# Optimization experiments

Hardware: AMD Instinct MI355X
Metric: run time of the kernel (lower is better)

Reference implementation:

```python
import jax, jax.numpy as jnp
import numpy as np

H = 1024   # hidden_size
A = 16     # number_ab (branches)
O = 4      # num_outputs per branch
B = 4096   # batch
P = 2048   # number of selected rows
EPS = 1e-5


def setup_inputs() -> dict:
    key = jax.random.key(0)
    ks = jax.random.split(key, 12)
    s = 0.02  # weight init scale
    inp = {
        "X": jax.random.normal(ks[0], (B, H), jnp.float32),
        "X1": jax.random.normal(ks[1], (B, H), jnp.float32),
        # stacked per-branch parameters (batched over antibody axis A)
        "W1": jax.random.normal(ks[2], (A, H, H), jnp.float32) * s,
        "b1": jnp.zeros((A, H), jnp.float32),
        "W2": jax.random.normal(ks[3], (A, H, H), jnp.float32) * s,
        "b2": jnp.zeros((A, H), jnp.float32),
        "W3": jax.random.normal(ks[4], (A, H, H), jnp.float32) * s,
        "b3": jnp.zeros((A, H), jnp.float32),
        "gamma": jnp.ones((A, H), jnp.float32),
        "beta": jnp.zeros((A, H), jnp.float32),
        "W4": jax.random.normal(ks[5], (A, H, O), jnp.float32) * s,
        "b4": jnp.zeros((A, O), jnp.float32),
        "positions_y": jax.random.randint(ks[6], (P,), 0, B, jnp.int32),
    }
    return inp


def reference(X, X1, W1, b1, W2, b2, W3, b3, gamma, beta, W4, b4, positions_y):
    # z = l1(X) + l2(X1) per branch, batched over A: [B, A, H]
    z = (jnp.einsum('bh,aho->bao', X, W1) + b1
         + jnp.einsum('bh,aho->bao', X1, W2) + b2)
    # mlm: Linear -> ReLU -> LayerNorm -> Linear
    h = jax.nn.relu(jnp.einsum('bah,aho->bao', z, W3) + b3)  # [B, A, H]
    mu = jnp.mean(h, axis=-1, keepdims=True)
    var = jnp.var(h, axis=-1, keepdims=True)  # biased, matches nn.LayerNorm
    hn = (h - mu) / jnp.sqrt(var + EPS) * gamma + beta
    y = jnp.einsum('bah,aho->bao', hn, W4) + b4  # [B, A, O]
    # torch.cat along dim 1 over branches -> [B, A*O]
    Y = y.reshape(B, A * O)
    return Y[positions_y]
```

## Files before the change

### kernel.cpp

```cpp
#include <hip/hip_runtime.h>
#include <hip/hip_bf16.h>

using bf16 = __hip_bfloat16;
typedef __bf16 v8bf __attribute__((ext_vector_type(8)));
typedef float v4f __attribute__((ext_vector_type(4)));

#define H_ 1024
#define A_ 16
#define O_ 4
#define B_ 4096
#define P_ 2048
#define EPS_ 1e-5f

__device__ __forceinline__ void gl_lds16(const void* g, void* l) {
    __builtin_amdgcn_global_load_lds(
        (const __attribute__((address_space(1))) void*)g,
        (__attribute__((address_space(3))) void*)l, 16, 0, 0);
}

__global__ void addbias_k(const float* __restrict__ b1, const float* __restrict__ b2,
                          float* __restrict__ b12, int n) {
    int i = blockIdx.x * 256 + threadIdx.x;
    if (i < n) b12[i] = b1[i] + b2[i];
}

__global__ __launch_bounds__(256) void gather_k(const float* __restrict__ X,
                                                const float* __restrict__ X1,
                                                const int* __restrict__ pos,
                                                bf16* __restrict__ XX) {
    int p = blockIdx.x;
    int row = pos[p];
    const float4* x  = (const float4*)(X  + (size_t)row * H_);
    const float4* x1 = (const float4*)(X1 + (size_t)row * H_);
    bf16* o = XX + (size_t)p * (2 * H_);
    int i = threadIdx.x;
    float4 v = x[i];
    __align__(8) bf16 t[4];
    t[0] = __float2bfloat16(v.x); t[1] = __float2bfloat16(v.y);
    t[2] = __float2bfloat16(v.z); t[3] = __float2bfloat16(v.w);
    *(uint2*)(o + i * 4) = *(const uint2*)t;
    float4 w = x1[i];
    t[0] = __float2bfloat16(w.x); t[1] = __float2bfloat16(w.y);
    t[2] = __float2bfloat16(w.z); t[3] = __float2bfloat16(w.w);
    *(uint2*)(o + H_ + i * 4) = *(const uint2*)t;
}

__global__ __launch_bounds__(256) void transpose3_k(const float* __restrict__ W1s,
                                                    const float* __restrict__ W2s,
                                                    const float* __restrict__ W3s,
                                                    bf16* __restrict__ WT12,
                                                    bf16* __restrict__ WT3) {
    __shared__ float tile[64][65];
    const int which = blockIdx.z >> 4;
    const int a = blockIdx.z & 15;
    const float* src = (which == 0) ? W1s : (which == 1) ? W2s : W3s;
    bf16* dstBase = (which == 2) ? WT3 : WT12;
    const int dstK = (which == 2) ? H_ : 2 * H_;
    const int kOff = (which == 1) ? H_ : 0;

    const int k0 = blockIdx.x * 64;
    const int n0 = blockIdx.y * 64;
    const float* s = src + (size_t)a * H_ * H_;
    const int tc = threadIdx.x & 15;
    const int tr = threadIdx.x >> 4;
#pragma unroll
    for (int r = 0; r < 64; r += 16) {
        float4 v = *(const float4*)(s + (size_t)(k0 + tr + r) * H_ + n0 + tc * 4);
        tile[tr + r][tc * 4 + 0] = v.x;
        tile[tr + r][tc * 4 + 1] = v.y;
        tile[tr + r][tc * 4 + 2] = v.z;
        tile[tr + r][tc * 4 + 3] = v.w;
    }
    __syncthreads();
    bf16* d = dstBase + (size_t)a * H_ * dstK + kOff;
    const int wc = threadIdx.x & 7;
    const int wr = threadIdx.x >> 3;
#pragma unroll
    for (int r = 0; r < 64; r += 32) {
        const int n = wr + r;
        __align__(16) bf16 tmp[8];
#pragma unroll
        for (int j = 0; j < 8; j++) tmp[j] = __float2bfloat16(tile[wc * 8 + j][n]);
        *(uint4*)(d + (size_t)(n0 + n) * dstK + k0 + wc * 8) = *(const uint4*)tmp;
    }
}

template <bool RELU>
__global__ __launch_bounds__(256) void gemm_bt(const bf16* __restrict__ Amat, size_t aStrideA,
                                               const bf16* __restrict__ Bt,
                                               const float* __restrict__ bias,
                                               bf16* __restrict__ C,
                                               int M, int N, int K) {
    constexpr int BM = 128, BN = 128, BK = 32;
    __shared__ __align__(16) unsigned short As[2 * BM * BK];
    __shared__ __align__(16) unsigned short Bs[2 * BN * BK];

    const int L = blockIdx.x + 16 * blockIdx.y + 128 * blockIdx.z;
    const int xcd = L & 7;
    const int g = L >> 3;
    const int bm = g & 15;
    const int bna = xcd + 8 * (g >> 4);
    const int bn = bna & 7;
    const int a = bna >> 3;

    const bf16* Ab = Amat + (size_t)a * aStrideA;
    const bf16* Bb = Bt + (size_t)a * (size_t)N * K;
    const int tid = threadIdx.x;
    const int lane = tid & 63;
    const int wave = tid >> 6;
    const int wm = (wave & 1) * 64;
    const int wn = (wave >> 1) * 64;

    v4f acc[4][4];
#pragma unroll
    for (int i = 0; i < 4; i++)
#pragma unroll
        for (int j = 0; j < 4; j++) acc[i][j] = (v4f){0.f, 0.f, 0.f, 0.f};

    const int r0 = tid >> 2;
    const int cs = (((tid & 3) ^ ((r0 >> 1) & 3))) * 8;
    const bf16* agBase = Ab + (size_t)(bm * BM + r0) * K + cs;
    const bf16* bgBase = Bb + (size_t)(bn * BN + r0) * K + cs;
    const size_t rowSkip = (size_t)64 * K;
    const int w512 = wave * 512;

    const int lr = lane & 15;
    const int q = lane >> 4;
    const int kq = (q ^ ((lr >> 1) & 3)) * 8;

    const int nk = K / BK;

    {
        unsigned short* aB = As;
        unsigned short* bB = Bs;
        gl_lds16(agBase, aB + w512);
        gl_lds16(agBase + rowSkip, aB + 2048 + w512);
        gl_lds16(bgBase, bB + w512);
        gl_lds16(bgBase + rowSkip, bB + 2048 + w512);
    }

    for (int kt = 0; kt < nk; ++kt) {
        __syncthreads();
        if (kt + 1 < nk) {
            const int k0 = (kt + 1) * BK;
            unsigned short* aB = As + ((kt + 1) & 1) * 4096;
            unsigned short* bB = Bs + ((kt + 1) & 1) * 4096;
            gl_lds16(agBase + k0, aB + w512);
            gl_lds16(agBase + k0 + rowSkip, aB + 2048 + w512);
            gl_lds16(bgBase + k0, bB + w512);
            gl_lds16(bgBase + k0 + rowSkip, bB + 2048 + w512);
        }
        const unsigned short* Ar = As + (kt & 1) * 4096;
        const unsigned short* Br = Bs + (kt & 1) * 4096;
        v8bf af[4], bfr[4];
#pragma unroll
        for (int mi = 0; mi < 4; mi++)
            af[mi] = *(const v8bf*)(Ar + (wm + mi * 16 + lr) * BK + kq);
#pragma unroll
        for (int ni = 0; ni < 4; ni++)
            bfr[ni] = *(const v8bf*)(Br + (wn + ni * 16 + lr) * BK + kq);
#pragma unroll
        for (int mi = 0; mi < 4; mi++)
#pragma unroll
            for (int ni = 0; ni < 4; ni++)
                acc[mi][ni] = __builtin_amdgcn_mfma_f32_16x16x32_bf16(af[mi], bfr[ni],
                                                                      acc[mi][ni], 0, 0, 0);
    }

    const int lq = lane >> 4;
    bf16* Cb = C + (size_t)a * M * N;
#pragma unroll
    for (int ni = 0; ni < 4; ni++) {
        const int col = bn * BN + wn + ni * 16 + lr;
        const float bv = bias[(size_t)a * N + col];
#pragma unroll
        for (int mi = 0; mi < 4; mi++) {
            const int row0 = bm * BM + wm + mi * 16 + lq * 4;
#pragma unroll
            for (int rg = 0; rg < 4; rg++) {
                float v = acc[mi][ni][rg] + bv;
                if (RELU) v = v > 0.f ? v : 0.f;
                Cb[(size_t)(row0 + rg) * N + col] = __float2bfloat16(v);
            }
        }
    }
}

__global__ __launch_bounds__(256) void ln_head_k(const bf16* __restrict__ Hb,
                                                 const float* __restrict__ gamma,
                                                 const float* __restrict__ beta,
                                                 const float* __restrict__ W4,
                                                 const float* __restrict__ b4,
                                                 float* __restrict__ out) {
    int w = blockIdx.x * 4 + (threadIdx.x >> 6);
    int lane = threadIdx.x & 63;
    int a = w >> 11;
    int p = w & (P_ - 1);
    const bf16* hrow = Hb + ((size_t)a * P_ + p) * H_;
    float hv[16];
    float s = 0.f, ss = 0.f;
#pragma unroll
    for (int i = 0; i < 16; i++) {
        float v = __bfloat162float(hrow[lane + i * 64]);
        hv[i] = v;
        s += v;
        ss += v * v;
    }
#pragma unroll
    for (int off = 32; off; off >>= 1) {
        s += __shfl_xor(s, off);
        ss += __shfl_xor(ss, off);
    }
    float mu = s * (1.f / H_);
    float var = ss * (1.f / H_) - mu * mu;
    float rstd = rsqrtf(var + EPS_);
    const float* g = gamma + (size_t)a * H_;
    const float* be = beta + (size_t)a * H_;
    const float4* w4 = (const float4*)(W4 + (size_t)a * H_ * O_);
    float a0 = 0.f, a1 = 0.f, a2 = 0.f, a3 = 0.f;
#pragma unroll
    for (int i = 0; i < 16; i++) {
        int k = lane + i * 64;
        float hn = (hv[i] - mu) * rstd * g[k] + be[k];
        float4 wv = w4[k];
        a0 += hn * wv.x;
        a1 += hn * wv.y;
        a2 += hn * wv.z;
        a3 += hn * wv.w;
    }
#pragma unroll
    for (int off = 32; off; off >>= 1) {
        a0 += __shfl_xor(a0, off);
        a1 += __shfl_xor(a1, off);
        a2 += __shfl_xor(a2, off);
        a3 += __shfl_xor(a3, off);
    }
    if (lane < 4) {
        float v = (lane == 0 ? a0 : lane == 1 ? a1 : lane == 2 ? a2 : a3) + b4[a * O_ + lane];
        out[(size_t)p * (A_ * O_) + a * O_ + lane] = v;
    }
}

extern "C" void kernel_launch(void* const* d_in, const int* in_sizes, int n_in,
                              void* d_out, int out_size, void* d_ws, size_t ws_size,
                              hipStream_t stream) {
    const float* X     = (const float*)d_in[0];
    const float* X1    = (const float*)d_in[1];
    const float* W1    = (const float*)d_in[2];
    const float* b1    = (const float*)d_in[3];
    const float* W2    = (const float*)d_in[4];
    const float* b2    = (const float*)d_in[5];
    const float* W3    = (const float*)d_in[6];
    const float* b3    = (const float*)d_in[7];
    const float* gamma = (const float*)d_in[8];
    const float* beta  = (const float*)d_in[9];
    const float* W4    = (const float*)d_in[10];
    const float* b4    = (const float*)d_in[11];
    const int* pos     = (const int*)d_in[12];
    float* out = (float*)d_out;

    char* ws = (char*)d_ws;
    bf16* XX   = (bf16*)(ws);
    bf16* Z    = (bf16*)(ws + ((size_t)8 << 20));
    bf16* WT3  = (bf16*)(ws + ((size_t)72 << 20));
    bf16* WT12 = (bf16*)(ws + ((size_t)104 << 20));
    float* b12 = (float*)(ws + ((size_t)168 << 20));
    bf16* Hb   = WT12;

    addbias_k<<<(A_ * H_ + 255) / 256, 256, 0, stream>>>(b1, b2, b12, A_ * H_);
    gather_k<<<P_, 256, 0, stream>>>(X, X1, pos, XX);
    dim3 tgrid(H_ / 64, H_ / 64, 3 * A_);
    transpose3_k<<<tgrid, 256, 0, stream>>>(W1, W2, W3, WT12, WT3);

    dim3 g1(P_ / 128, H_ / 128, A_);
    gemm_bt<false><<<g1, 256, 0, stream>>>(XX, 0, WT12, b12, Z, P_, H_, 2 * H_);
    gemm_bt<true><<<g1, 256, 0, stream>>>(Z, (size_t)P_ * H_, WT3, b3, Hb, P_, H_, H_);

    ln_head_k<<<P_ * A_ / 4, 256, 0, stream>>>(Hb, gamma, beta, W4, b4, out);
}
```

Baseline: 527.3 us.

## Merge bias add into gather, template GEMM on K, vectorize LN head loads

Folds the bias-sum kernel into the gather kernel as extra blocks, removing one launch. Makes the GEMM K dimension a template constant and unrolls the k-loop by 4, so the compiler can fold address math. Changes the LayerNorm head to read 8 bf16 values per lane with vector loads and vector-load gamma/beta. The LN element mapping changes to contiguous per-lane chunks; W4 reads stay scalar float4 per element.

```diff
diff --git a/kernel.cpp b/kernel.cpp
--- a/kernel.cpp
+++ b/kernel.cpp
@@ -18,16 +18,18 @@
         (__attribute__((address_space(3))) void*)l, 16, 0, 0);
 }
 
-__global__ void addbias_k(const float* __restrict__ b1, const float* __restrict__ b2,
-                          float* __restrict__ b12, int n) {
-    int i = blockIdx.x * 256 + threadIdx.x;
-    if (i < n) b12[i] = b1[i] + b2[i];
-}
-
-__global__ __launch_bounds__(256) void gather_k(const float* __restrict__ X,
-                                                const float* __restrict__ X1,
-                                                const int* __restrict__ pos,
-                                                bf16* __restrict__ XX) {
+__global__ __launch_bounds__(256) void gather_bias_k(const float* __restrict__ X,
+                                                     const float* __restrict__ X1,
+                                                     const int* __restrict__ pos,
+                                                     bf16* __restrict__ XX,
+                                                     const float* __restrict__ b1,
+                                                     const float* __restrict__ b2,
+                                                     float* __restrict__ b12) {
+    if (blockIdx.x >= P_) {
+        int i = (blockIdx.x - P_) * 256 + threadIdx.x;
+        if (i < A_ * H_) b12[i] = b1[i] + b2[i];
+        return;
+    }
     int p = blockIdx.x;
     int row = pos[p];
     const float4* x  = (const float4*)(X  + (size_t)row * H_);
@@ -85,13 +87,14 @@
     }
 }
 
-template <bool RELU>
+template <int K, bool RELU>
 __global__ __launch_bounds__(256) void gemm_bt(const bf16* __restrict__ Amat, size_t aStrideA,
                                                const bf16* __restrict__ Bt,
                                                const float* __restrict__ bias,
                                                bf16* __restrict__ C,
-                                               int M, int N, int K) {
+                                               int M, int N) {
     constexpr int BM = 128, BN = 128, BK = 32;
+    constexpr int NK = K / BK;
     __shared__ __align__(16) unsigned short As[2 * BM * BK];
     __shared__ __align__(16) unsigned short Bs[2 * BN * BK];
 
@@ -121,27 +124,22 @@
     const int cs = (((tid & 3) ^ ((r0 >> 1) & 3))) * 8;
     const bf16* agBase = Ab + (size_t)(bm * BM + r0) * K + cs;
     const bf16* bgBase = Bb + (size_t)(bn * BN + r0) * K + cs;
-    const size_t rowSkip = (size_t)64 * K;
+    constexpr size_t rowSkip = (size_t)64 * K;
     const int w512 = wave * 512;
 
     const int lr = lane & 15;
     const int q = lane >> 4;
     const int kq = (q ^ ((lr >> 1) & 3)) * 8;
 
-    const int nk = K / BK;
-
-    {
-        unsigned short* aB = As;
-        unsigned short* bB = Bs;
-        gl_lds16(agBase, aB + w512);
-        gl_lds16(agBase + rowSkip, aB + 2048 + w512);
-        gl_lds16(bgBase, bB + w512);
-        gl_lds16(bgBase + rowSkip, bB + 2048 + w512);
-    }
-
-    for (int kt = 0; kt < nk; ++kt) {
+    gl_lds16(agBase, As + w512);
+    gl_lds16(agBase + rowSkip, As + 2048 + w512);
+    gl_lds16(bgBase, Bs + w512);
+    gl_lds16(bgBase + rowSkip, Bs + 2048 + w512);
+
+#pragma unroll 4
+    for (int kt = 0; kt < NK; ++kt) {
         __syncthreads();
-        if (kt + 1 < nk) {
+        if (kt + 1 < NK) {
             const int k0 = (kt + 1) * BK;
             unsigned short* aB = As + ((kt + 1) & 1) * 4096;
             unsigned short* bB = Bs + ((kt + 1) & 1) * 4096;
@@ -197,14 +195,19 @@
     int a = w >> 11;
     int p = w & (P_ - 1);
     const bf16* hrow = Hb + ((size_t)a * P_ + p) * H_;
+    v8bf hv0 = *(const v8bf*)(hrow + lane * 8);
+    v8bf hv1 = *(const v8bf*)(hrow + 512 + lane * 8);
     float hv[16];
     float s = 0.f, ss = 0.f;
 #pragma unroll
-    for (int i = 0; i < 16; i++) {
-        float v = __bfloat162float(hrow[lane + i * 64]);
-        hv[i] = v;
-        s += v;
-        ss += v * v;
+    for (int j = 0; j < 8; j++) {
+        float v = (float)hv0[j];
+        hv[j] = v; s += v; ss += v * v;
+    }
+#pragma unroll
+    for (int j = 0; j < 8; j++) {
+        float v = (float)hv1[j];
+        hv[8 + j] = v; s += v; ss += v * v;
     }
 #pragma unroll
     for (int off = 32; off; off >>= 1) {
@@ -219,14 +222,24 @@
     const float4* w4 = (const float4*)(W4 + (size_t)a * H_ * O_);
     float a0 = 0.f, a1 = 0.f, a2 = 0.f, a3 = 0.f;
 #pragma unroll
-    for (int i = 0; i < 16; i++) {
-        int k = lane + i * 64;
-        float hn = (hv[i] - mu) * rstd * g[k] + be[k];
-        float4 wv = w4[k];
-        a0 += hn * wv.x;
-        a1 += hn * wv.y;
-        a2 += hn * wv.z;
-        a3 += hn * wv.w;
+    for (int half = 0; half < 2; half++) {
+        const int kb = half * 512 + lane * 8;
+        const float4 g4a = *(const float4*)(g + kb);
+        const float4 g4b = *(const float4*)(g + kb + 4);
+        const float4 b4a = *(const float4*)(be + kb);
+        const float4 b4b = *(const float4*)(be + kb + 4);
+        const float gv[8] = {g4a.x, g4a.y, g4a.z, g4a.w, g4b.x, g4b.y, g4b.z, g4b.w};
+        const float bv[8] = {b4a.x, b4a.y, b4a.z, b4a.w, b4b.x, b4b.y, b4b.z, b4b.w};
+#pragma unroll
+        for (int j = 0; j < 8; j++) {
+            const int k = kb + j;
+            float hn = (hv[half * 8 + j] - mu) * rstd * gv[j] + bv[j];
+            float4 wv = w4[k];
+            a0 += hn * wv.x;
+            a1 += hn * wv.y;
+            a2 += hn * wv.z;
+            a3 += hn * wv.w;
+        }
     }
 #pragma unroll
     for (int off = 32; off; off >>= 1) {
@@ -267,14 +280,13 @@
     float* b12 = (float*)(ws + ((size_t)168 << 20));
     bf16* Hb   = WT12;
 
-    addbias_k<<<(A_ * H_ + 255) / 256, 256, 0, stream>>>(b1, b2, b12, A_ * H_);
-    gather_k<<<P_, 256, 0, stream>>>(X, X1, pos, XX);
+    gather_bias_k<<<P_ + 64, 256, 0, stream>>>(X, X1, pos, XX, b1, b2, b12);
     dim3 tgrid(H_ / 64, H_ / 64, 3 * A_);
     transpose3_k<<<tgrid, 256, 0, stream>>>(W1, W2, W3, WT12, WT3);
 
     dim3 g1(P_ / 128, H_ / 128, A_);
-    gemm_bt<false><<<g1, 256, 0, stream>>>(XX, 0, WT12, b12, Z, P_, H_, 2 * H_);
-    gemm_bt<true><<<g1, 256, 0, stream>>>(Z, (size_t)P_ * H_, WT3, b3, Hb, P_, H_, H_);
+    gemm_bt<2 * H_, false><<<g1, 256, 0, stream>>>(XX, 0, WT12, b12, Z, P_, H_);
+    gemm_bt<H_, true><<<g1, 256, 0, stream>>>(Z, (size_t)P_ * H_, WT3, b3, Hb, P_, H_);
 
     ln_head_k<<<P_ * A_ / 4, 256, 0, stream>>>(Hb, gamma, beta, W4, b4, out);
 }
```

Result: slower. 639.6 us (+21.3%).
